# Kernel optimization log

Measured on AMD Instinct MI355X. Metric: run time of the kernel, lower is better.

## Reference

```python
import jax, jax.numpy as jnp
import numpy as np

L_MAX = 3
MP_SCALING = 0.1
E = 640000
N_ATOMS = 20000
K = 32


def setup_inputs() -> dict:
    key = jax.random.key(0)
    k1, k2, k3, k4, k5 = jax.random.split(key, 5)
    sh = jax.random.normal(k1, (E, (L_MAX + 1) ** 2), dtype=jnp.float32)
    radial_basis = jax.random.normal(k2, (E, L_MAX + 1, K), dtype=jnp.float32)
    center_embedding = jax.random.normal(k3, (N_ATOMS, K), dtype=jnp.float32)
    centers = jax.random.randint(k4, (E,), 0, N_ATOMS, dtype=jnp.int32)
    neighbors = jax.random.randint(k5, (E,), 0, N_ATOMS, dtype=jnp.int32)
    return {
        "sh": sh,
        "radial_basis": radial_basis,
        "center_embedding": center_embedding,
        "centers": centers,
        "neighbors": neighbors,
        "n_atoms": N_ATOMS,
    }


def reference(sh, radial_basis, center_embedding, centers, neighbors, n_atoms):
    # Gather neighbor embeddings once: [E, K]
    emb_n = center_embedding[neighbors]
    blocks = []
    off = 0
    for l in range(L_MAX + 1):
        m = 2 * l + 1
        sh_l = sh[:, off:off + m]            # [E, m]
        off += m
        rb_l = radial_basis[:, l, :]          # [E, K]
        # edge-wise product sh * radial * gathered embedding: [E, m, K]
        src = sh_l[:, :, None] * (rb_l * emb_n)[:, None, :]
        # scatter-add over center atoms -> per-atom density [n_atoms, m, K]
        dens_l = jax.ops.segment_sum(src, centers, num_segments=n_atoms)
        blocks.append(dens_l * MP_SCALING)
    # concatenate per-l blocks along the component axis: [n_atoms, sum(2l+1)=16, K]
    return jnp.concatenate(blocks, axis=1)
```

## Files before the change

kernel.cpp:

```cpp
#include <hip/hip_runtime.h>

#define KDIM 32


__global__ void hist_kernel(const int* __restrict__ centers, int* __restrict__ counts, int n) {
    int i = blockIdx.x * blockDim.x + threadIdx.x;
    if (i < n) atomicAdd(&counts[centers[i]], 1);
}

__global__ __launch_bounds__(1024) void scan_kernel(const int* __restrict__ counts,
                                                    int* __restrict__ offsets,
                                                    int* __restrict__ cursor, int n) {
    __shared__ int lds[1024];
    int t = threadIdx.x;
    int chunk = (n + 1023) >> 10;
    int s = t * chunk;
    int e = min(s + chunk, n);
    int sum = 0;
    for (int i = s; i < e; i++) sum += counts[i];
    lds[t] = sum;
    __syncthreads();
    for (int off = 1; off < 1024; off <<= 1) {
        int v = (t >= off) ? lds[t - off] : 0;
        __syncthreads();
        lds[t] += v;
        __syncthreads();
    }
    int run = lds[t] - sum;
    for (int i = s; i < e; i++) {
        int c = counts[i];
        offsets[i] = run;
        cursor[i] = run;
        run += c;
    }
    if (t == 1023) offsets[n] = run;
}

__global__ void scatter_kernel(const int* __restrict__ centers,
                               const int* __restrict__ neighbors,
                               int* __restrict__ cursor,
                               int2* __restrict__ recs, int n) {
    int i = blockIdx.x * blockDim.x + threadIdx.x;
    if (i < n) {
        int c = centers[i];
        int nn = neighbors[i];
        int pos = atomicAdd(&cursor[c], 1);
        recs[pos] = make_int2(i, nn);
    }
}


#define EDGE_BODY(EB, RP, SHP)                                            \
    {                                                                     \
        float t0 = RP[0 * KDIM + k] * EB;                                 \
        float t1 = RP[1 * KDIM + k] * EB;                                 \
        float t2 = RP[2 * KDIM + k] * EB;                                 \
        float t3 = RP[3 * KDIM + k] * EB;                                 \
        float4 sA = SHP[0];                                               \
        float4 sB = SHP[1];                                               \
        float c0 = hb ? t2 : t0;                                          \
        float c1 = hb ? t3 : t1;                                          \
        float c2 = hb ? t3 : t2;                                          \
        a0 += sA.x * c0;                                                  \
        a1 += sA.y * c1;                                                  \
        a2 += sA.z * c1;                                                  \
        a3 += sA.w * c1;                                                  \
        a4 += sB.x * c2;                                                  \
        a5 += sB.y * c2;                                                  \
        a6 += sB.z * c2;                                                  \
        a7 += sB.w * c2;                                                  \
    }

__global__ __launch_bounds__(256) void imp_main_kernel(
    const float* __restrict__ sh, const float* __restrict__ rb,
    const float* __restrict__ emb, const int2* __restrict__ recs,
    const int* __restrict__ offsets, float* __restrict__ out, int n_atoms) {
    int wave = (blockIdx.x * blockDim.x + threadIdx.x) >> 6;
    int lane = threadIdx.x & 63;
    if (wave >= n_atoms) return;
    int k = lane & 31;
    int h = lane >> 5;
    bool hb = (h != 0);

    int start = offsets[wave];
    int end   = offsets[wave + 1];

    float a0 = 0.f, a1 = 0.f, a2 = 0.f, a3 = 0.f;
    float a4 = 0.f, a5 = 0.f, a6 = 0.f, a7 = 0.f;

    int i = start;
    for (; i + 4 <= end; i += 4) {
        int2 r0 = recs[i + 0];
        int2 r1 = recs[i + 1];
        int2 r2 = recs[i + 2];
        int2 r3 = recs[i + 3];
        int e0 = __builtin_amdgcn_readfirstlane(r0.x);
        int n0 = __builtin_amdgcn_readfirstlane(r0.y);
        int e1 = __builtin_amdgcn_readfirstlane(r1.x);
        int n1 = __builtin_amdgcn_readfirstlane(r1.y);
        int e2 = __builtin_amdgcn_readfirstlane(r2.x);
        int n2 = __builtin_amdgcn_readfirstlane(r2.y);
        int e3 = __builtin_amdgcn_readfirstlane(r3.x);
        int n3 = __builtin_amdgcn_readfirstlane(r3.y);

        float eb0 = emb[(size_t)n0 * KDIM + k];
        float eb1 = emb[(size_t)n1 * KDIM + k];
        float eb2 = emb[(size_t)n2 * KDIM + k];
        float eb3 = emb[(size_t)n3 * KDIM + k];

        const float* rp0 = rb + (size_t)e0 * (4 * KDIM);
        const float* rp1 = rb + (size_t)e1 * (4 * KDIM);
        const float* rp2 = rb + (size_t)e2 * (4 * KDIM);
        const float* rp3 = rb + (size_t)e3 * (4 * KDIM);

        const float4* sp0 = (const float4*)(sh + (size_t)e0 * 16 + 8 * h);
        const float4* sp1 = (const float4*)(sh + (size_t)e1 * 16 + 8 * h);
        const float4* sp2 = (const float4*)(sh + (size_t)e2 * 16 + 8 * h);
        const float4* sp3 = (const float4*)(sh + (size_t)e3 * 16 + 8 * h);

        EDGE_BODY(eb0, rp0, sp0)
        EDGE_BODY(eb1, rp1, sp1)
        EDGE_BODY(eb2, rp2, sp2)
        EDGE_BODY(eb3, rp3, sp3)
    }
    for (; i < end; i++) {
        int2 r0 = recs[i];
        int e0 = __builtin_amdgcn_readfirstlane(r0.x);
        int n0 = __builtin_amdgcn_readfirstlane(r0.y);
        float eb0 = emb[(size_t)n0 * KDIM + k];
        const float* rp0 = rb + (size_t)e0 * (4 * KDIM);
        const float4* sp0 = (const float4*)(sh + (size_t)e0 * 16 + 8 * h);
        EDGE_BODY(eb0, rp0, sp0)
    }

    const float SCALE = 0.1f;
    float* op = out + (size_t)wave * (16 * KDIM) + (size_t)(8 * h) * KDIM + k;
    op[0 * KDIM] = a0 * SCALE;
    op[1 * KDIM] = a1 * SCALE;
    op[2 * KDIM] = a2 * SCALE;
    op[3 * KDIM] = a3 * SCALE;
    op[4 * KDIM] = a4 * SCALE;
    op[5 * KDIM] = a5 * SCALE;
    op[6 * KDIM] = a6 * SCALE;
    op[7 * KDIM] = a7 * SCALE;
}

extern "C" void kernel_launch(void* const* d_in, const int* in_sizes, int n_in,
                              void* d_out, int out_size, void* d_ws, size_t ws_size,
                              hipStream_t stream) {
    const float* sh        = (const float*)d_in[0];
    const float* rb        = (const float*)d_in[1];
    const float* emb       = (const float*)d_in[2];
    const int*   centers   = (const int*)d_in[3];
    const int*   neighbors = (const int*)d_in[4];

    int E = in_sizes[3];
    int N = in_sizes[2] / KDIM;

    float* out = (float*)d_out;

    int2* recs    = (int2*)d_ws;
    int*  counts  = (int*)(recs + E);
    int*  offsets = counts + N;
    int*  cursor  = offsets + N + 1;

    hipMemsetAsync(counts, 0, (size_t)N * sizeof(int), stream);

    hist_kernel<<<(E + 255) / 256, 256, 0, stream>>>(centers, counts, E);
    scan_kernel<<<1, 1024, 0, stream>>>(counts, offsets, cursor, N);
    scatter_kernel<<<(E + 255) / 256, 256, 0, stream>>>(centers, neighbors, cursor, recs, E);

    int blocks = (N * 64 + 255) / 256;
    imp_main_kernel<<<blocks, 256, 0, stream>>>(sh, rb, emb, recs, offsets, out, N);
}
```

Measured before the change: 606.2 us.

## Replace global-atomic CSR build with range-partitioned LDS histogram and scatter

The histogram and scatter passes now give each block a fixed range of 157 atoms. Every block streams the whole centers (and neighbors) array with int4 loads and counts and places only its own atoms using LDS atomics, so the global atomics, the memset and the separate cursor array go away. The trade is that every block re-reads the full index arrays, which adds a lot of redundant L2 traffic. Only about 128 blocks launch, so parallelism in these passes is limited. A side effect is that edges within each atom come out more ordered, which may improve locality in the main gather kernel.

```diff
diff --git a/kernel.cpp b/kernel.cpp
--- a/kernel.cpp
+++ b/kernel.cpp
@@ -1,16 +1,38 @@
 #include <hip/hip_runtime.h>
 
 #define KDIM 32
-
-
-__global__ void hist_kernel(const int* __restrict__ centers, int* __restrict__ counts, int n) {
-    int i = blockIdx.x * blockDim.x + threadIdx.x;
-    if (i < n) atomicAdd(&counts[centers[i]], 1);
+#define RMAX 157
+#define T_PRE 512
+
+
+__global__ __launch_bounds__(T_PRE) void range_hist(const int* __restrict__ centers,
+                                                    int* __restrict__ counts,
+                                                    int n_atoms, int E) {
+    __shared__ int hist[RMAX];
+    int lo = blockIdx.x * RMAX;
+    int hi = min(lo + RMAX, n_atoms);
+    for (int j = threadIdx.x; j + lo < hi; j += blockDim.x) hist[j] = 0;
+    __syncthreads();
+
+    const int4* c4 = (const int4*)centers;
+    int nv = E >> 2;
+    for (int i = threadIdx.x; i < nv; i += blockDim.x) {
+        int4 c = c4[i];
+        if (c.x >= lo && c.x < hi) atomicAdd(&hist[c.x - lo], 1);
+        if (c.y >= lo && c.y < hi) atomicAdd(&hist[c.y - lo], 1);
+        if (c.z >= lo && c.z < hi) atomicAdd(&hist[c.z - lo], 1);
+        if (c.w >= lo && c.w < hi) atomicAdd(&hist[c.w - lo], 1);
+    }
+    for (int i = (nv << 2) + threadIdx.x; i < E; i += blockDim.x) {
+        int c = centers[i];
+        if (c >= lo && c < hi) atomicAdd(&hist[c - lo], 1);
+    }
+    __syncthreads();
+    for (int j = threadIdx.x; j + lo < hi; j += blockDim.x) counts[lo + j] = hist[j];
 }
 
 __global__ __launch_bounds__(1024) void scan_kernel(const int* __restrict__ counts,
-                                                    int* __restrict__ offsets,
-                                                    int* __restrict__ cursor, int n) {
+                                                    int* __restrict__ offsets, int n) {
     __shared__ int lds[1024];
     int t = threadIdx.x;
     int chunk = (n + 1023) >> 10;
@@ -30,22 +52,37 @@
     for (int i = s; i < e; i++) {
         int c = counts[i];
         offsets[i] = run;
-        cursor[i] = run;
         run += c;
     }
     if (t == 1023) offsets[n] = run;
 }
 
-__global__ void scatter_kernel(const int* __restrict__ centers,
-                               const int* __restrict__ neighbors,
-                               int* __restrict__ cursor,
-                               int2* __restrict__ recs, int n) {
-    int i = blockIdx.x * blockDim.x + threadIdx.x;
-    if (i < n) {
+__global__ __launch_bounds__(T_PRE) void range_scatter(const int* __restrict__ centers,
+                                                       const int* __restrict__ neighbors,
+                                                       const int* __restrict__ offsets,
+                                                       int2* __restrict__ recs,
+                                                       int n_atoms, int E) {
+    __shared__ int cur[RMAX];
+    int lo = blockIdx.x * RMAX;
+    int hi = min(lo + RMAX, n_atoms);
+    for (int j = threadIdx.x; j + lo < hi; j += blockDim.x) cur[j] = offsets[lo + j];
+    __syncthreads();
+
+    const int4* c4 = (const int4*)centers;
+    const int4* n4 = (const int4*)neighbors;
+    int nv = E >> 2;
+    for (int i = threadIdx.x; i < nv; i += blockDim.x) {
+        int4 c = c4[i];
+        int4 nn = n4[i];
+        int base = i << 2;
+        if (c.x >= lo && c.x < hi) { int p = atomicAdd(&cur[c.x - lo], 1); recs[p] = make_int2(base + 0, nn.x); }
+        if (c.y >= lo && c.y < hi) { int p = atomicAdd(&cur[c.y - lo], 1); recs[p] = make_int2(base + 1, nn.y); }
+        if (c.z >= lo && c.z < hi) { int p = atomicAdd(&cur[c.z - lo], 1); recs[p] = make_int2(base + 2, nn.z); }
+        if (c.w >= lo && c.w < hi) { int p = atomicAdd(&cur[c.w - lo], 1); recs[p] = make_int2(base + 3, nn.w); }
+    }
+    for (int i = (nv << 2) + threadIdx.x; i < E; i += blockDim.x) {
         int c = centers[i];
-        int nn = neighbors[i];
-        int pos = atomicAdd(&cursor[c], 1);
-        recs[pos] = make_int2(i, nn);
+        if (c >= lo && c < hi) { int p = atomicAdd(&cur[c - lo], 1); recs[p] = make_int2(i, neighbors[i]); }
     }
 }
 
@@ -162,13 +199,12 @@
     int2* recs    = (int2*)d_ws;
     int*  counts  = (int*)(recs + E);
     int*  offsets = counts + N;
-    int*  cursor  = offsets + N + 1;
-
-    hipMemsetAsync(counts, 0, (size_t)N * sizeof(int), stream);
-
-    hist_kernel<<<(E + 255) / 256, 256, 0, stream>>>(centers, counts, E);
-    scan_kernel<<<1, 1024, 0, stream>>>(counts, offsets, cursor, N);
-    scatter_kernel<<<(E + 255) / 256, 256, 0, stream>>>(centers, neighbors, cursor, recs, E);
+
+    int B = (N + RMAX - 1) / RMAX;
+
+    range_hist<<<B, T_PRE, 0, stream>>>(centers, counts, N, E);
+    scan_kernel<<<1, 1024, 0, stream>>>(counts, offsets, N);
+    range_scatter<<<B, T_PRE, 0, stream>>>(centers, neighbors, offsets, recs, N, E);
 
     int blocks = (N * 64 + 255) / 256;
     imp_main_kernel<<<blocks, 256, 0, stream>>>(sh, rb, emb, recs, offsets, out, N);
```

Measured after the change: 851.3 us. 1.4x slower.
